# Kernel tuning notes

Hardware: AMD Instinct MI355X
Metric: run time of the kernel (lower is better)

The kernel has to match this reference:

```python
import jax, jax.numpy as jnp
import numpy as np

B, S, L, D, H, DH, DFF, V = 16, 512, 12, 512, 8, 64, 2048, 631
MAX_KLEN = 1024  # tgt_len + mem_len


def _ln(x, g, b, eps=1e-5):
    m = x.mean(-1, keepdims=True)
    v = ((x - m) ** 2).mean(-1, keepdims=True)
    return (x - m) / jnp.sqrt(v + eps) * g + b


def _rot_half(x):
    # interleaved pair rotation: (x0,x1,x2,x3,..) -> (-x1,x0,-x3,x2,..)
    xe = x[..., ::2]
    xo = x[..., 1::2]
    return jnp.stack((-xo, xe), axis=-1).reshape(x.shape)


def _sin_cos(seq_len, d_head):
    inv_freq = 1.0 / 10000.0 ** (jnp.arange(0, d_head, 2, dtype=jnp.float32) / d_head)
    t = jnp.arange(seq_len, dtype=jnp.float32)[:, None] * inv_freq[None, :]
    sin = jnp.repeat(jnp.sin(t), 2, axis=-1)  # (S, DH)
    cos = jnp.repeat(jnp.cos(t), 2, axis=-1)
    return sin, cos


def setup_inputs() -> dict:
    key = jax.random.key(0)
    ks = jax.random.split(key, 12)
    std = 0.02
    data = jax.random.randint(ks[0], (B, S), 0, V)
    emb = jax.random.normal(ks[1], (V, D), jnp.float32) * std
    pos = jax.random.normal(ks[2], (MAX_KLEN, D), jnp.float32) * std
    Wq = jax.random.normal(ks[3], (L, D, H * DH), jnp.float32) * std
    Wkv = jax.random.normal(ks[4], (L, D, 2 * H * DH), jnp.float32) * std
    Wo = jax.random.normal(ks[5], (L, H * DH, D), jnp.float32) * std
    W1 = jax.random.normal(ks[6], (L, D, DFF), jnp.float32) * std
    b1 = jnp.zeros((L, DFF), jnp.float32)
    W2 = jax.random.normal(ks[7], (L, DFF, D), jnp.float32) * std
    b2 = jnp.zeros((L, D), jnp.float32)
    ln1_g = jnp.ones((L, D), jnp.float32)
    ln1_b = jnp.zeros((L, D), jnp.float32)
    ln2_g = jnp.ones((L, D), jnp.float32)
    ln2_b = jnp.zeros((L, D), jnp.float32)
    out_b = jnp.zeros((V,), jnp.float32)
    return dict(data=data, emb=emb, pos=pos, Wq=Wq, Wkv=Wkv, Wo=Wo,
                W1=W1, b1=b1, W2=W2, b2=b2,
                ln1_g=ln1_g, ln1_b=ln1_b, ln2_g=ln2_g, ln2_b=ln2_b, out_b=out_b)


def reference(data, emb, pos, Wq, Wkv, Wo, W1, b1, W2, b2,
              ln1_g, ln1_b, ln2_g, ln2_b, out_b):
    sin, cos = _sin_cos(S, DH)
    sin = sin[None, :, None, :]  # (1,S,1,DH) broadcast over (B,S,H,DH)
    cos = cos[None, :, None, :]
    causal = jnp.triu(jnp.ones((S, S), bool), 1)
    scale = 1.0 / jnp.sqrt(jnp.float32(DH))

    h = emb[data] + pos[:S][None]  # (B,S,D)
    for l in range(L):
        q = (h @ Wq[l]).reshape(B, S, H, DH)
        kv = h @ Wkv[l]
        k = kv[..., :H * DH].reshape(B, S, H, DH)
        v = kv[..., H * DH:].reshape(B, S, H, DH)
        q = q * cos + _rot_half(q) * sin
        k = k * cos + _rot_half(k) * sin
        sc = jnp.einsum('bqhd,bkhd->bhqk', q, k) * scale
        sc = jnp.where(causal[None, None], -jnp.inf, sc)
        p = jax.nn.softmax(sc, axis=-1)
        av = jnp.einsum('bhqk,bkhd->bqhd', p, v).reshape(B, S, H * DH)
        h = _ln(h + av @ Wo[l], ln1_g[l], ln1_b[l])
        ff = jax.nn.relu(h @ W1[l] + b1[l]) @ W2[l] + b2[l]
        h = _ln(h + ff, ln2_g[l], ln2_b[l])
    # tied output projection: out_layer.weight = word_emb.weight, plus bias
    return h @ emb.T + out_b
```

## Files before the change

### kernel.cpp

```cpp
#include <hip/hip_runtime.h>
#include <hip/hip_bf16.h>

typedef __hip_bfloat16 bf16;
typedef __attribute__((ext_vector_type(8))) short short8;
typedef __attribute__((ext_vector_type(4))) float f32x4;

static constexpr int Bz = 16, Sq = 512, Lw = 12, Dm = 512, Hh = 8, DFFd = 2048, Vv = 631;
static constexpr int Mtok = Bz * Sq;
static constexpr int VPAD = 640;
static constexpr int QKS = 1024;

__device__ __forceinline__ bf16 f2b(float x) { return __float2bfloat16(x); }
__device__ __forceinline__ float bfu(unsigned short s) {
    union { unsigned u; float f; } c; c.u = (unsigned)s << 16; return c.f;
}

__device__ __forceinline__ f32x4 z4() { f32x4 v; v[0]=0.f; v[1]=0.f; v[2]=0.f; v[3]=0.f; return v; }

__device__ __forceinline__ void gload_lds16(const bf16* g, bf16* l) {
    __builtin_amdgcn_global_load_lds(
        (const __attribute__((address_space(1))) unsigned int*)(g),
        (__attribute__((address_space(3))) unsigned int*)(l),
        16, 0, 0);
}

__global__ void k_sincos(float* __restrict__ cosT, float* __restrict__ sinT) {
    int i = blockIdx.x * 256 + threadIdx.x;
    int s = i >> 5, f = i & 31;
    float inv = powf(10000.0f, -(float)(2 * f) / 64.0f);
    float t = (float)s * inv;
    sinT[i] = sinf(t);
    cosT[i] = cosf(t);
}

__global__ void k_embconv(const float* __restrict__ emb, bf16* __restrict__ embT) {
    int i = blockIdx.x * 256 + threadIdx.x;
    int n = i >> 9;
    embT[i] = (n < Vv) ? f2b(emb[i]) : f2b(0.0f);
}

__global__ void k_embed(const int* __restrict__ data, const float* __restrict__ emb,
                        const float* __restrict__ pos, float* __restrict__ hf, bf16* __restrict__ hb) {
    int tok = blockIdx.x;
    int id = data[tok];
    int s = tok & (Sq - 1);
    for (int d = threadIdx.x; d < Dm; d += 256) {
        float v = emb[id * Dm + d] + pos[s * Dm + d];
        hf[(size_t)tok * Dm + d] = v;
        hb[(size_t)tok * Dm + d] = f2b(v);
    }
}

__global__ void k_wtrans(const float* __restrict__ src, bf16* __restrict__ dst,
                         int K, int N, long long sStride, long long dStride) {
    src += (long long)blockIdx.z * sStride;
    dst += (long long)blockIdx.z * dStride;
    __shared__ float tile[32][33];
    int k0 = blockIdx.y * 32, n0 = blockIdx.x * 32;
    int tx = threadIdx.x & 31, ty = threadIdx.x >> 5;
    #pragma unroll
    for (int r = ty; r < 32; r += 8) tile[r][tx] = src[(size_t)(k0 + r) * N + n0 + tx];
    __syncthreads();
    #pragma unroll
    for (int r = ty; r < 32; r += 8) dst[(size_t)(n0 + r) * K + k0 + tx] = f2b(tile[tx][r]);
}

template<int EPI>
__global__ __launch_bounds__(512) void k_gemmW(const bf16* __restrict__ A, const bf16* __restrict__ Bt,
                                               void* __restrict__ Cout, void* __restrict__ Cout2,
                                               const float* __restrict__ bias,
                                               const float* __restrict__ cosT, const float* __restrict__ sinT,
                                               int M, int N, int K, int ldA, int ldB) {
    extern __shared__ __align__(16) char smem[];
    bf16* lAbase = (bf16*)smem;
    bf16* lBbase = (bf16*)(smem + 3 * 256 * 32 * 2);

    const int t = threadIdx.x;
    const int lane = t & 63;
    const int wave = t >> 6;
    const int wr = wave >> 1, wc = wave & 1;
    const int l15 = lane & 15, l4 = lane >> 4;

    const int gx = gridDim.x, gy = gridDim.y;
    const int nwg = gx * gy * gridDim.z;
    const int cpx = nwg >> 3;
    int lin = (blockIdx.z * gy + blockIdx.y) * gx + blockIdx.x;
    lin = (lin & 7) * cpx + (lin >> 3);
    const int bn = lin % gx;
    const int rem = lin / gx;
    const int bm = rem % gy;
    const int bz = rem / gy;

    const bf16* Ab = A + (size_t)(bm * 256) * ldA + (size_t)bz * K;
    const bf16* Bb = Bt + (size_t)(bn * 128) * ldB + (size_t)bz * K;

    int soffA[2], soffB0;
    #pragma unroll
    for (int p = 0; p < 2; p++) {
        int q = p * 512 + t, r = q >> 2, s = q & 3;
        soffA[p] = r * ldA + ((s ^ ((r >> 1) & 3)) << 3);
    }
    {
        int r = t >> 2, s = t & 3;
        soffB0 = r * ldB + ((s ^ ((r >> 1) & 3)) << 3);
    }

    f32x4 acc[4][4];
    #pragma unroll
    for (int i = 0; i < 4; i++)
        #pragma unroll
        for (int j = 0; j < 4; j++) acc[i][j] = z4();

    auto STAGE = [&](int buf, int kt) {
        const int k0 = kt << 5;
        bf16* la = lAbase + buf * (256 * 32);
        bf16* lb = lBbase + buf * (128 * 32);
        #pragma unroll
        for (int p = 0; p < 2; p++)
            gload_lds16(Ab + (size_t)soffA[p] + k0, &la[(p * 512 + t) * 8]);
        gload_lds16(Bb + (size_t)soffB0 + k0, &lb[t * 8]);
    };

    auto COMPUTE = [&](int buf) {
        const char* la = (const char*)(lAbase + buf * (256 * 32));
        const char* lb = (const char*)(lBbase + buf * (128 * 32));
        short8 af[4], bfr[4];
        #pragma unroll
        for (int i = 0; i < 4; i++) {
            int row = wr * 64 + i * 16 + l15;
            af[i] = *(const short8*)(la + row * 64 + (((l4 ^ (row >> 1)) & 3) << 4));
        }
        #pragma unroll
        for (int j = 0; j < 4; j++) {
            int row = wc * 64 + j * 16 + l15;
            bfr[j] = *(const short8*)(lb + row * 64 + (((l4 ^ (row >> 1)) & 3) << 4));
        }
        #pragma unroll
        for (int i = 0; i < 4; i++)
            #pragma unroll
            for (int j = 0; j < 4; j++)
                acc[i][j] = __builtin_amdgcn_mfma_f32_16x16x32_bf16(af[i], bfr[j], acc[i][j], 0, 0, 0);
    };

    const int nk = K >> 5;
    STAGE(0, 0);
    STAGE(1, 1);
    int kt = 0;
    for (; kt < nk - 1; ++kt) {
        asm volatile("s_waitcnt vmcnt(3)" ::: "memory");
        __builtin_amdgcn_s_barrier();
        if (kt + 2 < nk) STAGE((kt + 2) % 3, kt + 2);
        __builtin_amdgcn_s_setprio(1);
        COMPUTE(kt % 3);
        __builtin_amdgcn_s_setprio(0);
    }
    asm volatile("s_waitcnt vmcnt(0)" ::: "memory");
    __builtin_amdgcn_s_barrier();
    __builtin_amdgcn_s_setprio(1);
    COMPUTE(kt % 3);
    __builtin_amdgcn_s_setprio(0);

    #pragma unroll
    for (int i = 0; i < 4; i++) {
        #pragma unroll
        for (int j = 0; j < 4; j++) {
            const int col = bn * 128 + wc * 64 + j * 16 + l15;
            const int row0 = bm * 256 + wr * 64 + i * 16 + l4 * 4;
            if (EPI == 4 && col >= 1024) {
                int h = (col - 1024) >> 6, d = (col - 1024) & 63;
                int b = row0 >> 9, s0 = row0 & 511;
                bf16 pk[4];
                #pragma unroll
                for (int r = 0; r < 4; r++) pk[r] = f2b(acc[i][j][r]);
                *(ushort4*)&((bf16*)Cout2)[((size_t)(b * 8 + h) * 64 + d) * 512 + s0] =
                    *(const ushort4*)pk;
                continue;
            }
            #pragma unroll
            for (int r = 0; r < 4; r++) {
                int row = row0 + r;
                float v = acc[i][j][r];
                if (EPI == 1) {
                    bf16* Co = (bf16*)(bz ? Cout2 : Cout);
                    Co[(size_t)row * N + col] = f2b(v);
                } else if (EPI == 2) {
                    v += bias[col];
                    v = v > 0.f ? v : 0.f;
                    ((bf16*)Cout)[(size_t)row * N + col] = f2b(v);
                } else if (EPI == 3) {
                    if (col < Vv) ((float*)Cout)[(size_t)row * Vv + col] = v + bias[col];
                } else {
                    float p = __shfl_xor(v, 1, 64);
                    int srow = row & (Sq - 1);
                    int f = (col >> 1) & 31;
                    float cc = cosT[srow * 32 + f], sn = sinT[srow * 32 + f];
                    float o = (col & 1) ? (v * cc + p * sn) : (v * cc - p * sn);
                    if (col < 512) o *= 0.125f;
                    ((bf16*)Cout)[(size_t)row * QKS + col] = f2b(o);
                }
            }
        }
    }
}

__global__ __launch_bounds__(512) void k_attn(const bf16* __restrict__ qkv,
                                              const bf16* __restrict__ vt, bf16* __restrict__ av) {
    __shared__ __align__(16) bf16 lK[2][64][80];
    __shared__ __align__(16) bf16 lV[2][64][80];
    __shared__ __align__(16) bf16 lP[8][16][88];
    const int tq = blockIdx.x, bh = blockIdx.y;
    const int b = bh >> 3, h = bh & 7;
    const int t = threadIdx.x, lane = t & 63, w = t >> 6;
    const int l15 = lane & 15, l4 = lane >> 4;
    const int q0 = tq * 128;
    const int rowb = q0 + w * 16;

    short8 qf[2];
    {
        const bf16* qr = qkv + (size_t)(b * Sq + rowb + l15) * QKS + h * 64 + l4 * 8;
        qf[0] = *(const short8*)qr;
        qf[1] = *(const short8*)(qr + 32);
    }
    f32x4 o[4];
    #pragma unroll
    for (int j = 0; j < 4; j++) o[j] = z4();
    float mrow[4] = {-1e30f, -1e30f, -1e30f, -1e30f};
    float ssum[4] = {0.f, 0.f, 0.f, 0.f};

    const int nk = (q0 >> 6) + 2;
    const int sr = t >> 3, scc = (t & 7) * 8;
    const bf16* gK = qkv + (size_t)(b * Sq + sr) * QKS + 512 + h * 64 + scc;
    const bf16* gV = vt + (size_t)(bh * 64 + sr) * 512 + scc;
    uint4 rK = *(const uint4*)gK;
    uint4 rV = *(const uint4*)gV;

    for (int kt = 0; kt < nk; ++kt) {
        const int buf = kt & 1;
        const int kv0 = kt * 64;
        uint4 nK, nV;
        if (kt + 1 < nk) {
            nK = *(const uint4*)(gK + (size_t)(kt + 1) * 64 * QKS);
            nV = *(const uint4*)(gV + (size_t)(kt + 1) * 64);
        }
        *(uint4*)&lK[buf][sr][scc] = rK;
        *(uint4*)&lV[buf][sr][scc] = rV;
        asm volatile("s_waitcnt lgkmcnt(0)" ::: "memory");
        __builtin_amdgcn_s_barrier();
        __builtin_amdgcn_sched_barrier(0);

        if (kv0 <= rowb + 15) {
            f32x4 sc[4];
            #pragma unroll
            for (int j = 0; j < 4; j++) sc[j] = z4();
            #pragma unroll
            for (int j = 0; j < 4; j++)
                #pragma unroll
                for (int ks = 0; ks < 2; ks++) {
                    short8 kf = *(const short8*)&lK[buf][j * 16 + l15][ks * 32 + l4 * 8];
                    sc[j] = __builtin_amdgcn_mfma_f32_16x16x32_bf16(qf[ks], kf, sc[j], 0, 0, 0);
                }
            if (kv0 + 63 > rowb) {
                #pragma unroll
                for (int j = 0; j < 4; j++)
                    #pragma unroll
                    for (int r = 0; r < 4; r++)
                        if (kv0 + j * 16 + l15 > rowb + l4 * 4 + r) sc[j][r] = -1e30f;
            }
            float corr[4];
            #pragma unroll
            for (int r = 0; r < 4; r++) {
                float m_ = fmaxf(fmaxf(sc[0][r], sc[1][r]), fmaxf(sc[2][r], sc[3][r]));
                #pragma unroll
                for (int d = 1; d < 16; d <<= 1) m_ = fmaxf(m_, __shfl_xor(m_, d, 64));
                float mo = mrow[r];
                float mn = fmaxf(mo, m_);
                mrow[r] = mn;
                corr[r] = __expf(mo - mn);
            }
            float p[4][4];
            #pragma unroll
            for (int j = 0; j < 4; j++)
                #pragma unroll
                for (int r = 0; r < 4; r++)
                    p[j][r] = __expf(sc[j][r] - mrow[r]);
            #pragma unroll
            for (int r = 0; r < 4; r++)
                ssum[r] = ssum[r] * corr[r] + p[0][r] + p[1][r] + p[2][r] + p[3][r];
            #pragma unroll
            for (int j = 0; j < 4; j++)
                #pragma unroll
                for (int r = 0; r < 4; r++)
                    lP[w][l4 * 4 + r][j * 16 + l15] = f2b(p[j][r]);
            #pragma unroll
            for (int j = 0; j < 4; j++) {
                o[j][0] *= corr[0]; o[j][1] *= corr[1]; o[j][2] *= corr[2]; o[j][3] *= corr[3];
            }
            #pragma unroll
            for (int ks = 0; ks < 2; ks++) {
                short8 pa = *(const short8*)&lP[w][l15][ks * 32 + l4 * 8];
                #pragma unroll
                for (int j = 0; j < 4; j++) {
                    short8 vb = *(const short8*)&lV[buf][j * 16 + l15][ks * 32 + l4 * 8];
                    o[j] = __builtin_amdgcn_mfma_f32_16x16x32_bf16(pa, vb, o[j], 0, 0, 0);
                }
            }
        }
        rK = nK; rV = nV;
    }
    #pragma unroll
    for (int r = 0; r < 4; r++) {
        float s = ssum[r];
        #pragma unroll
        for (int d = 1; d < 16; d <<= 1) s += __shfl_xor(s, d, 64);
        ssum[r] = 1.f / s;
    }
    #pragma unroll
    for (int j = 0; j < 4; j++)
        #pragma unroll
        for (int r = 0; r < 4; r++)
            av[(size_t)(b * Sq + rowb + l4 * 4 + r) * 512 + h * 64 + j * 16 + l15] = f2b(o[j][r] * ssum[r]);
}

template<bool ADDB>
__global__ __launch_bounds__(256) void k_addln(float* __restrict__ hf, bf16* __restrict__ hb,
                                               const bf16* __restrict__ d1, const bf16* __restrict__ d2,
                                               const float* __restrict__ bias,
                                               const float* __restrict__ gamma, const float* __restrict__ beta) {
    const int lane = threadIdx.x & 63, w = threadIdx.x >> 6;
    const int row = blockIdx.x * 4 + w;
    const size_t base = (size_t)row * Dm + lane * 8;
    float v[8];
    float4 h0 = *(const float4*)&hf[base];
    float4 h1 = *(const float4*)&hf[base + 4];
    short8 a8 = *(const short8*)&d1[base];
    short8 b8 = *(const short8*)&d2[base];
    v[0] = h0.x; v[1] = h0.y; v[2] = h0.z; v[3] = h0.w;
    v[4] = h1.x; v[5] = h1.y; v[6] = h1.z; v[7] = h1.w;
    #pragma unroll
    for (int k = 0; k < 8; k++)
        v[k] += bfu((unsigned short)a8[k]) + bfu((unsigned short)b8[k]);
    if (ADDB) {
        float4 bb0 = *(const float4*)&bias[lane * 8];
        float4 bb1 = *(const float4*)&bias[lane * 8 + 4];
        v[0] += bb0.x; v[1] += bb0.y; v[2] += bb0.z; v[3] += bb0.w;
        v[4] += bb1.x; v[5] += bb1.y; v[6] += bb1.z; v[7] += bb1.w;
    }
    float s = 0.f, sq = 0.f;
    #pragma unroll
    for (int k = 0; k < 8; k++) { s += v[k]; sq += v[k] * v[k]; }
    #pragma unroll
    for (int m = 1; m < 64; m <<= 1) { s += __shfl_xor(s, m, 64); sq += __shfl_xor(sq, m, 64); }
    float mean = s * (1.f / Dm);
    float var = sq * (1.f / Dm) - mean * mean;
    float inv = rsqrtf(var + 1e-5f);
    float4 g0 = *(const float4*)&gamma[lane * 8];
    float4 g1 = *(const float4*)&gamma[lane * 8 + 4];
    float4 e0 = *(const float4*)&beta[lane * 8];
    float4 e1 = *(const float4*)&beta[lane * 8 + 4];
    float gs[8] = {g0.x, g0.y, g0.z, g0.w, g1.x, g1.y, g1.z, g1.w};
    float es[8] = {e0.x, e0.y, e0.z, e0.w, e1.x, e1.y, e1.z, e1.w};
    float ov[8];
    short8 ob;
    #pragma unroll
    for (int k = 0; k < 8; k++) {
        ov[k] = (v[k] - mean) * inv * gs[k] + es[k];
        ob[k] = (short)__bfloat16_as_ushort(f2b(ov[k]));
    }
    float4 o0; o0.x = ov[0]; o0.y = ov[1]; o0.z = ov[2]; o0.w = ov[3];
    float4 o1; o1.x = ov[4]; o1.y = ov[5]; o1.z = ov[6]; o1.w = ov[7];
    *(float4*)&hf[base] = o0;
    *(float4*)&hf[base + 4] = o1;
    *(short8*)&hb[base] = ob;
}

extern "C" void kernel_launch(void* const* d_in, const int* in_sizes, int n_in,
                              void* d_out, int out_size, void* d_ws, size_t ws_size,
                              hipStream_t stream) {
    const int*   data = (const int*)d_in[0];
    const float* emb  = (const float*)d_in[1];
    const float* pos  = (const float*)d_in[2];
    const float* Wq   = (const float*)d_in[3];
    const float* Wkv  = (const float*)d_in[4];
    const float* Wo   = (const float*)d_in[5];
    const float* W1   = (const float*)d_in[6];
    const float* b1   = (const float*)d_in[7];
    const float* W2   = (const float*)d_in[8];
    const float* b2   = (const float*)d_in[9];
    const float* ln1g = (const float*)d_in[10];
    const float* ln1b = (const float*)d_in[11];
    const float* ln2g = (const float*)d_in[12];
    const float* ln2b = (const float*)d_in[13];
    const float* outb = (const float*)d_in[14];
    float* out = (float*)d_out;
    char* ws = (char*)d_ws;

    const int WLDS = 3 * (256 * 32 + 128 * 32) * 2;
    (void)hipFuncSetAttribute((const void*)&k_gemmW<1>, hipFuncAttributeMaxDynamicSharedMemorySize, WLDS);
    (void)hipFuncSetAttribute((const void*)&k_gemmW<2>, hipFuncAttributeMaxDynamicSharedMemorySize, WLDS);
    (void)hipFuncSetAttribute((const void*)&k_gemmW<3>, hipFuncAttributeMaxDynamicSharedMemorySize, WLDS);
    (void)hipFuncSetAttribute((const void*)&k_gemmW<4>, hipFuncAttributeMaxDynamicSharedMemorySize, WLDS);

    size_t off = 0;
    auto take = [&](size_t bytes) { size_t r = off; off += (bytes + 255) & ~(size_t)255; return r; };
    float* hf    = (float*)(ws + take((size_t)Mtok * Dm * 4));
    bf16*  hb    = (bf16*)(ws + take((size_t)Mtok * Dm * 2));
    bf16*  qkvbf = (bf16*)(ws + take((size_t)Mtok * QKS * 2));
    bf16*  vtb   = (bf16*)(ws + take((size_t)Mtok * Dm * 2));
    bf16*  avb   = (bf16*)(ws + take((size_t)Mtok * Dm * 2));
    bf16*  tmpb  = (bf16*)(ws + take((size_t)Mtok * Dm * 2));
    bf16*  tmp2b = (bf16*)(ws + take((size_t)Mtok * Dm * 2));
    bf16*  ff1   = (bf16*)(ws + take((size_t)Mtok * DFFd * 2));
    float* cosT  = (float*)(ws + take((size_t)Sq * 32 * 4));
    float* sinT  = (float*)(ws + take((size_t)Sq * 32 * 4));
    bf16*  embT  = (bf16*)(ws + take((size_t)VPAD * Dm * 2));

    const size_t ofsQKV = 0;
    const size_t ofsO   = ofsQKV + (size_t)1536 * 512;
    const size_t ofsW1  = ofsO + (size_t)512 * 512;
    const size_t ofsW2  = ofsW1 + (size_t)512 * 2048;
    const size_t SLABE  = ofsW2 + (size_t)2048 * 512;

    bf16* wT = (bf16*)(ws + off);
    size_t remain = (ws_size > off) ? (ws_size - off) : 0;
    bool upfront = remain >= SLABE * 12 * 2;

    k_sincos<<<(Sq * 32) / 256, 256, 0, stream>>>(cosT, sinT);
    k_embconv<<<(VPAD * Dm) / 256, 256, 0, stream>>>(emb, embT);
    k_embed<<<Mtok, 256, 0, stream>>>(data, emb, pos, hf, hb);

    if (upfront) {
        k_wtrans<<<dim3(16, 16, 12), 256, 0, stream>>>(Wq,  wT + ofsQKV,             512, 512,  (long long)512 * 512,  (long long)SLABE);
        k_wtrans<<<dim3(32, 16, 12), 256, 0, stream>>>(Wkv, wT + ofsQKV + 512 * 512, 512, 1024, (long long)512 * 1024, (long long)SLABE);
        k_wtrans<<<dim3(16, 16, 12), 256, 0, stream>>>(Wo,  wT + ofsO,  512, 512,  (long long)512 * 512,  (long long)SLABE);
        k_wtrans<<<dim3(64, 16, 12), 256, 0, stream>>>(W1,  wT + ofsW1, 512, 2048, (long long)512 * 2048, (long long)SLABE);
        k_wtrans<<<dim3(16, 64, 12), 256, 0, stream>>>(W2,  wT + ofsW2, 2048, 512, (long long)2048 * 512, (long long)SLABE);
    }

    for (int l = 0; l < Lw; l++) {
        bf16* slab = wT + (upfront ? (size_t)l * SLABE : 0);
        if (!upfront) {
            k_wtrans<<<dim3(16, 16, 1), 256, 0, stream>>>(Wq  + (size_t)l * 512 * 512,  slab + ofsQKV,             512, 512,  0, 0);
            k_wtrans<<<dim3(32, 16, 1), 256, 0, stream>>>(Wkv + (size_t)l * 512 * 1024, slab + ofsQKV + 512 * 512, 512, 1024, 0, 0);
            k_wtrans<<<dim3(16, 16, 1), 256, 0, stream>>>(Wo  + (size_t)l * 512 * 512,  slab + ofsO,  512, 512,  0, 0);
            k_wtrans<<<dim3(64, 16, 1), 256, 0, stream>>>(W1  + (size_t)l * 512 * 2048, slab + ofsW1, 512, 2048, 0, 0);
            k_wtrans<<<dim3(16, 64, 1), 256, 0, stream>>>(W2  + (size_t)l * 2048 * 512, slab + ofsW2, 2048, 512, 0, 0);
        }
        k_gemmW<4><<<dim3(12, 32, 1), 512, WLDS, stream>>>(hb, slab + ofsQKV, qkvbf, vtb, nullptr, cosT, sinT,
                                                           Mtok, 1536, 512, 512, 512);
        k_attn<<<dim3(4, 128), 512, 0, stream>>>(qkvbf, vtb, avb);
        k_gemmW<1><<<dim3(4, 32, 2), 512, WLDS, stream>>>(avb, slab + ofsO, tmpb, tmp2b, nullptr, nullptr, nullptr,
                                                          Mtok, 512, 256, 512, 512);
        k_addln<false><<<Mtok / 4, 256, 0, stream>>>(hf, hb, tmpb, tmp2b, nullptr,
                                                     ln1g + (size_t)l * Dm, ln1b + (size_t)l * Dm);
        k_gemmW<2><<<dim3(16, 32, 1), 512, WLDS, stream>>>(hb, slab + ofsW1, ff1, nullptr, b1 + (size_t)l * DFFd,
                                                           nullptr, nullptr, Mtok, 2048, 512, 512, 512);
        k_gemmW<1><<<dim3(4, 32, 2), 512, WLDS, stream>>>(ff1, slab + ofsW2, tmpb, tmp2b, nullptr, nullptr, nullptr,
                                                          Mtok, 512, 1024, 2048, 2048);
        k_addln<true><<<Mtok / 4, 256, 0, stream>>>(hf, hb, tmpb, tmp2b, b2 + (size_t)l * Dm,
                                                    ln2g + (size_t)l * Dm, ln2b + (size_t)l * Dm);
    }
    k_gemmW<3><<<dim3(5, 32, 1), 512, WLDS, stream>>>(hb, embT, out, nullptr, outb, nullptr, nullptr,
                                                      Mtok, VPAD, 512, 512, 512);
}
```

Before: 1.647 ms.

## Interleave LDS fragment reads, global prefetch and MFMA phases in GEMM main loop

```diff
diff --git a/kernel.cpp b/kernel.cpp
--- a/kernel.cpp
+++ b/kernel.cpp
@@ -149,9 +149,54 @@
     for (; kt < nk - 1; ++kt) {
         asm volatile("s_waitcnt vmcnt(3)" ::: "memory");
         __builtin_amdgcn_s_barrier();
-        if (kt + 2 < nk) STAGE((kt + 2) % 3, kt + 2);
+        const char* la = (const char*)(lAbase + (kt % 3) * (256 * 32));
+        const char* lb = (const char*)(lBbase + (kt % 3) * (128 * 32));
+        bf16* lan = lAbase + ((kt + 2) % 3) * (256 * 32);
+        bf16* lbn = lBbase + ((kt + 2) % 3) * (128 * 32);
+        const size_t k0n = (size_t)((kt + 2) << 5);
+        const bool st = (kt + 2 < nk);
+        short8 af[4], bfr[4];
+        auto RA = [&](int i) {
+            int row = wr * 64 + i * 16 + l15;
+            af[i] = *(const short8*)(la + row * 64 + (((l4 ^ (row >> 1)) & 3) << 4));
+        };
+        auto RB = [&](int j) {
+            int row = wc * 64 + j * 16 + l15;
+            bfr[j] = *(const short8*)(lb + row * 64 + (((l4 ^ (row >> 1)) & 3) << 4));
+        };
+        auto MM = [&](int i, int j) {
+            acc[i][j] = __builtin_amdgcn_mfma_f32_16x16x32_bf16(af[i], bfr[j], acc[i][j], 0, 0, 0);
+        };
+        RA(0); RA(1); RB(0); RB(1);
+        if (st) gload_lds16(Ab + (size_t)soffA[0] + k0n, &lan[t * 8]);
+        __builtin_amdgcn_sched_barrier(0);
+        __builtin_amdgcn_s_barrier();
+        __builtin_amdgcn_sched_barrier(0);
         __builtin_amdgcn_s_setprio(1);
-        COMPUTE(kt % 3);
+        MM(0, 0); MM(0, 1); MM(1, 0); MM(1, 1);
+        __builtin_amdgcn_s_setprio(0);
+        __builtin_amdgcn_sched_barrier(0);
+        __builtin_amdgcn_s_barrier();
+        __builtin_amdgcn_sched_barrier(0);
+        RB(2); RB(3);
+        if (st) gload_lds16(Ab + (size_t)soffA[1] + k0n, &lan[(512 + t) * 8]);
+        __builtin_amdgcn_sched_barrier(0);
+        __builtin_amdgcn_s_barrier();
+        __builtin_amdgcn_sched_barrier(0);
+        __builtin_amdgcn_s_setprio(1);
+        MM(0, 2); MM(0, 3); MM(1, 2); MM(1, 3);
+        __builtin_amdgcn_s_setprio(0);
+        __builtin_amdgcn_sched_barrier(0);
+        __builtin_amdgcn_s_barrier();
+        __builtin_amdgcn_sched_barrier(0);
+        RA(2); RA(3);
+        if (st) gload_lds16(Bb + (size_t)soffB0 + k0n, &lbn[t * 8]);
+        __builtin_amdgcn_sched_barrier(0);
+        __builtin_amdgcn_s_barrier();
+        __builtin_amdgcn_sched_barrier(0);
+        __builtin_amdgcn_s_setprio(1);
+        MM(2, 0); MM(2, 1); MM(3, 0); MM(3, 1);
+        MM(2, 2); MM(2, 3); MM(3, 2); MM(3, 3);
         __builtin_amdgcn_s_setprio(0);
     }
     asm volatile("s_waitcnt vmcnt(0)" ::: "memory");
```

Measured after the change: 1.657 ms. Within noise of the previous version (+0.6%).

## Fuse split-K reduction, residual add and LayerNorm into GEMM epilogue via counters

Applied to the files above, without the earlier changes.

```diff
diff --git a/kernel.cpp b/kernel.cpp
--- a/kernel.cpp
+++ b/kernel.cpp
@@ -9,6 +9,7 @@
 static constexpr int Mtok = Bz * Sq;
 static constexpr int VPAD = 640;
 static constexpr int QKS = 1024;
+static constexpr int NCNT = 24 * 32;
 
 __device__ __forceinline__ bf16 f2b(float x) { return __float2bfloat16(x); }
 __device__ __forceinline__ float bfu(unsigned short s) {
@@ -24,8 +25,9 @@
         16, 0, 0);
 }
 
-__global__ void k_sincos(float* __restrict__ cosT, float* __restrict__ sinT) {
+__global__ void k_sincos(float* __restrict__ cosT, float* __restrict__ sinT, int* __restrict__ cnt) {
     int i = blockIdx.x * 256 + threadIdx.x;
+    if (i < NCNT) cnt[i] = 0;
     int s = i >> 5, f = i & 31;
     float inv = powf(10000.0f, -(float)(2 * f) / 64.0f);
     float t = (float)s * inv;
@@ -70,7 +72,10 @@
                                                void* __restrict__ Cout, void* __restrict__ Cout2,
                                                const float* __restrict__ bias,
                                                const float* __restrict__ cosT, const float* __restrict__ sinT,
-                                               int M, int N, int K, int ldA, int ldB) {
+                                               int M, int N, int K, int ldA, int ldB,
+                                               float* __restrict__ hfp, bf16* __restrict__ hbp,
+                                               const float* __restrict__ gamma, const float* __restrict__ beta,
+                                               int* __restrict__ cnt) {
     extern __shared__ __align__(16) char smem[];
     bf16* lAbase = (bf16*)smem;
     bf16* lBbase = (bf16*)(smem + 3 * 256 * 32 * 2);
@@ -181,8 +186,7 @@
                 int row = row0 + r;
                 float v = acc[i][j][r];
                 if (EPI == 1) {
-                    bf16* Co = (bf16*)(bz ? Cout2 : Cout);
-                    Co[(size_t)row * N + col] = f2b(v);
+                    ((bf16*)Cout)[(size_t)bz * ((size_t)M * N) + (size_t)row * N + col] = f2b(v);
                 } else if (EPI == 2) {
                     v += bias[col];
                     v = v > 0.f ? v : 0.f;
@@ -201,6 +205,68 @@
             }
         }
     }
+
+    if (EPI == 1) {
+        __syncthreads();
+        if (t == 0) {
+            __hip_atomic_fetch_add(cnt + bm, 1, __ATOMIC_ACQ_REL, __HIP_MEMORY_SCOPE_AGENT);
+            while (__hip_atomic_load(cnt + bm, __ATOMIC_RELAXED, __HIP_MEMORY_SCOPE_AGENT) < 8)
+                __builtin_amdgcn_s_sleep(2);
+        }
+        __syncthreads();
+        __builtin_amdgcn_fence(__ATOMIC_ACQUIRE, "agent");
+        const bf16* part = (const bf16*)Cout;
+        const size_t pstr = (size_t)M * N;
+        const int wv = t >> 6, lx = t & 63;
+        const int r0 = bm * 256 + (bz * 4 + bn) * 32 + wv * 4;
+        #pragma unroll
+        for (int rr = 0; rr < 4; rr++) {
+            const int row = r0 + rr;
+            const size_t base = (size_t)row * N + lx * 8;
+            float v[8];
+            float4 h0 = *(const float4*)&hfp[base];
+            float4 h1 = *(const float4*)&hfp[base + 4];
+            short8 p0 = *(const short8*)&part[base];
+            short8 p1 = *(const short8*)&part[base + pstr];
+            v[0] = h0.x; v[1] = h0.y; v[2] = h0.z; v[3] = h0.w;
+            v[4] = h1.x; v[5] = h1.y; v[6] = h1.z; v[7] = h1.w;
+            #pragma unroll
+            for (int k = 0; k < 8; k++)
+                v[k] += bfu((unsigned short)p0[k]) + bfu((unsigned short)p1[k]);
+            if (bias) {
+                float4 b0 = *(const float4*)&bias[lx * 8];
+                float4 b1 = *(const float4*)&bias[lx * 8 + 4];
+                v[0] += b0.x; v[1] += b0.y; v[2] += b0.z; v[3] += b0.w;
+                v[4] += b1.x; v[5] += b1.y; v[6] += b1.z; v[7] += b1.w;
+            }
+            float s = 0.f, sq = 0.f;
+            #pragma unroll
+            for (int k = 0; k < 8; k++) { s += v[k]; sq += v[k] * v[k]; }
+            #pragma unroll
+            for (int m2 = 1; m2 < 64; m2 <<= 1) { s += __shfl_xor(s, m2, 64); sq += __shfl_xor(sq, m2, 64); }
+            float mean = s * (1.f / 512.f);
+            float var = sq * (1.f / 512.f) - mean * mean;
+            float inv = rsqrtf(var + 1e-5f);
+            float4 g0 = *(const float4*)&gamma[lx * 8];
+            float4 g1 = *(const float4*)&gamma[lx * 8 + 4];
+            float4 e0 = *(const float4*)&beta[lx * 8];
+            float4 e1 = *(const float4*)&beta[lx * 8 + 4];
+            float gs[8] = {g0.x, g0.y, g0.z, g0.w, g1.x, g1.y, g1.z, g1.w};
+            float es[8] = {e0.x, e0.y, e0.z, e0.w, e1.x, e1.y, e1.z, e1.w};
+            float ov[8];
+            short8 ob;
+            #pragma unroll
+            for (int k = 0; k < 8; k++) {
+                ov[k] = (v[k] - mean) * inv * gs[k] + es[k];
+                ob[k] = (short)__bfloat16_as_ushort(f2b(ov[k]));
+            }
+            float4 o0; o0.x = ov[0]; o0.y = ov[1]; o0.z = ov[2]; o0.w = ov[3];
+            float4 o1; o1.x = ov[4]; o1.y = ov[5]; o1.z = ov[6]; o1.w = ov[7];
+            *(float4*)&hfp[base] = o0;
+            *(float4*)&hfp[base + 4] = o1;
+            *(short8*)&hbp[base] = ob;
+        }
+    }
 }
 
 __global__ __launch_bounds__(512) void k_attn(const bf16* __restrict__ qkv,
@@ -319,58 +385,6 @@
         #pragma unroll
         for (int r = 0; r < 4; r++)
             av[(size_t)(b * Sq + rowb + l4 * 4 + r) * 512 + h * 64 + j * 16 + l15] = f2b(o[j][r] * ssum[r]);
-}
-
-template<bool ADDB>
-__global__ __launch_bounds__(256) void k_addln(float* __restrict__ hf, bf16* __restrict__ hb,
-                                               const bf16* __restrict__ d1, const bf16* __restrict__ d2,
-                                               const float* __restrict__ bias,
-                                               const float* __restrict__ gamma, const float* __restrict__ beta) {
-    const int lane = threadIdx.x & 63, w = threadIdx.x >> 6;
-    const int row = blockIdx.x * 4 + w;
-    const size_t base = (size_t)row * Dm + lane * 8;
-    float v[8];
-    float4 h0 = *(const float4*)&hf[base];
-    float4 h1 = *(const float4*)&hf[base + 4];
-    short8 a8 = *(const short8*)&d1[base];
-    short8 b8 = *(const short8*)&d2[base];
-    v[0] = h0.x; v[1] = h0.y; v[2] = h0.z; v[3] = h0.w;
-    v[4] = h1.x; v[5] = h1.y; v[6] = h1.z; v[7] = h1.w;
-    #pragma unroll
-    for (int k = 0; k < 8; k++)
-        v[k] += bfu((unsigned short)a8[k]) + bfu((unsigned short)b8[k]);
-    if (ADDB) {
-        float4 bb0 = *(const float4*)&bias[lane * 8];
-        float4 bb1 = *(const float4*)&bias[lane * 8 + 4];
-        v[0] += bb0.x; v[1] += bb0.y; v[2] += bb0.z; v[3] += bb0.w;
-        v[4] += bb1.x; v[5] += bb1.y; v[6] += bb1.z; v[7] += bb1.w;
-    }
-    float s = 0.f, sq = 0.f;
-    #pragma unroll
-    for (int k = 0; k < 8; k++) { s += v[k]; sq += v[k] * v[k]; }
-    #pragma unroll
-    for (int m = 1; m < 64; m <<= 1) { s += __shfl_xor(s, m, 64); sq += __shfl_xor(sq, m, 64); }
-    float mean = s * (1.f / Dm);
-    float var = sq * (1.f / Dm) - mean * mean;
-    float inv = rsqrtf(var + 1e-5f);
-    float4 g0 = *(const float4*)&gamma[lane * 8];
-    float4 g1 = *(const float4*)&gamma[lane * 8 + 4];
-    float4 e0 = *(const float4*)&beta[lane * 8];
-    float4 e1 = *(const float4*)&beta[lane * 8 + 4];
-    float gs[8] = {g0.x, g0.y, g0.z, g0.w, g1.x, g1.y, g1.z, g1.w};
-    float es[8] = {e0.x, e0.y, e0.z, e0.w, e1.x, e1.y, e1.z, e1.w};
-    float ov[8];
-    short8 ob;
-    #pragma unroll
-    for (int k = 0; k < 8; k++) {
-        ov[k] = (v[k] - mean) * inv * gs[k] + es[k];
-        ob[k] = (short)__bfloat16_as_ushort(f2b(ov[k]));
-    }
-    float4 o0; o0.x = ov[0]; o0.y = ov[1]; o0.z = ov[2]; o0.w = ov[3];
-    float4 o1; o1.x = ov[4]; o1.y = ov[5]; o1.z = ov[6]; o1.w = ov[7];
-    *(float4*)&hf[base] = o0;
-    *(float4*)&hf[base + 4] = o1;
-    *(short8*)&hb[base] = ob;
 }
 
 extern "C" void kernel_launch(void* const* d_in, const int* in_sizes, int n_in,
@@ -407,12 +421,12 @@
     bf16*  qkvbf = (bf16*)(ws + take((size_t)Mtok * QKS * 2));
     bf16*  vtb   = (bf16*)(ws + take((size_t)Mtok * Dm * 2));
     bf16*  avb   = (bf16*)(ws + take((size_t)Mtok * Dm * 2));
-    bf16*  tmpb  = (bf16*)(ws + take((size_t)Mtok * Dm * 2));
-    bf16*  tmp2b = (bf16*)(ws + take((size_t)Mtok * Dm * 2));
+    bf16*  part  = (bf16*)(ws + take((size_t)2 * Mtok * Dm * 2));
     bf16*  ff1   = (bf16*)(ws + take((size_t)Mtok * DFFd * 2));
     float* cosT  = (float*)(ws + take((size_t)Sq * 32 * 4));
     float* sinT  = (float*)(ws + take((size_t)Sq * 32 * 4));
     bf16*  embT  = (bf16*)(ws + take((size_t)VPAD * Dm * 2));
+    int*   cntb  = (int*)(ws + take((size_t)NCNT * 4));
 
     const size_t ofsQKV = 0;
     const size_t ofsO   = ofsQKV + (size_t)1536 * 512;
@@ -424,7 +438,7 @@
     size_t remain = (ws_size > off) ? (ws_size - off) : 0;
     bool upfront = remain >= SLABE * 12 * 2;
 
-    k_sincos<<<(Sq * 32) / 256, 256, 0, stream>>>(cosT, sinT);
+    k_sincos<<<(Sq * 32) / 256, 256, 0, stream>>>(cosT, sinT, cntb);
     k_embconv<<<(VPAD * Dm) / 256, 256, 0, stream>>>(emb, embT);
     k_embed<<<Mtok, 256, 0, stream>>>(data, emb, pos, hf, hb);
 
@@ -446,19 +460,22 @@
             k_wtrans<<<dim3(16, 64, 1), 256, 0, stream>>>(W2  + (size_t)l * 2048 * 512, slab + ofsW2, 2048, 512, 0, 0);
         }
         k_gemmW<4><<<dim3(12, 32, 1), 512, WLDS, stream>>>(hb, slab + ofsQKV, qkvbf, vtb, nullptr, cosT, sinT,
-                                                           Mtok, 1536, 512, 512, 512);
+                                                           Mtok, 1536, 512, 512, 512,
+                                                           nullptr, nullptr, nullptr, nullptr, nullptr);
         k_attn<<<dim3(4, 128), 512, 0, stream>>>(qkvbf, vtb, avb);
-        k_gemmW<1><<<dim3(4, 32, 2), 512, WLDS, stream>>>(avb, slab + ofsO, tmpb, tmp2b, nullptr, nullptr, nullptr,
-                                                          Mtok, 512, 256, 512, 512);
-        k_addln<false><<<Mtok / 4, 256, 0, stream>>>(hf, hb, tmpb, tmp2b, nullptr,
-                                                     ln1g + (size_t)l * Dm, ln1b + (size_t)l * Dm);
+        k_gemmW<1><<<dim3(4, 32, 2), 512, WLDS, stream>>>(avb, slab + ofsO, part, nullptr, nullptr, nullptr, nullptr,
+                                                          Mtok, 512, 256, 512, 512,
+                                                          hf, hb, ln1g + (size_t)l * Dm, ln1b + (size_t)l * Dm,
+                                                          cntb + (size_t)(l * 2) * 32);
         k_gemmW<2><<<dim3(16, 32, 1), 512, WLDS, stream>>>(hb, slab + ofsW1, ff1, nullptr, b1 + (size_t)l * DFFd,
-                                                           nullptr, nullptr, Mtok, 2048, 512, 512, 512);
-        k_gemmW<1><<<dim3(4, 32, 2), 512, WLDS, stream>>>(ff1, slab + ofsW2, tmpb, tmp2b, nullptr, nullptr, nullptr,
-                                                          Mtok, 512, 1024, 2048, 2048);
-        k_addln<true><<<Mtok / 4, 256, 0, stream>>>(hf, hb, tmpb, tmp2b, b2 + (size_t)l * Dm,
-                                                    ln2g + (size_t)l * Dm, ln2b + (size_t)l * Dm);
+                                                           nullptr, nullptr, Mtok, 2048, 512, 512, 512,
+                                                           nullptr, nullptr, nullptr, nullptr, nullptr);
+        k_gemmW<1><<<dim3(4, 32, 2), 512, WLDS, stream>>>(ff1, slab + ofsW2, part, nullptr, b2 + (size_t)l * Dm,
+                                                          nullptr, nullptr, Mtok, 512, 1024, 2048, 2048,
+                                                          hf, hb, ln2g + (size_t)l * Dm, ln2b + (size_t)l * Dm,
+                                                          cntb + (size_t)(l * 2 + 1) * 32);
     }
     k_gemmW<3><<<dim3(5, 32, 1), 512, WLDS, stream>>>(hb, embT, out, nullptr, outb, nullptr, nullptr,
-                                                      Mtok, VPAD, 512, 512, 512);
-}
+                                                      Mtok, VPAD, 512, 512, 512,
+                                                      nullptr, nullptr, nullptr, nullptr, nullptr);
+}
```

Measured after the change: 2.193 ms. 33.1% more time.
